# Performance work log

Hardware: AMD Instinct MI355X
Metric: run time of the kernel (lower is better)

## Reference

```python
import jax, jax.numpy as jnp
import numpy as np

N = 100_000
E = 1_000_000
D = 64
NORM_FACTOR = 100.0
LN_EPS = 1e-5


def setup_inputs() -> dict:
    key = jax.random.key(0)
    ks = jax.random.split(key, 8)
    h = jax.random.normal(ks[0], (N, D), dtype=jnp.float32)
    distances = jax.random.uniform(ks[1], (E, 1), dtype=jnp.float32)
    edges = jax.random.randint(ks[2], (2, E), 0, N, dtype=jnp.int64)
    node_mask = jnp.ones((N, 1), dtype=jnp.float32)
    edge_mask = jnp.ones((E, 1), dtype=jnp.float32)
    s = 1.0 / np.sqrt(D)
    W_lin = jax.random.normal(ks[3], (D, D), dtype=jnp.float32) * s
    b_lin = jnp.zeros((D,), dtype=jnp.float32)
    att_W1 = jax.random.normal(ks[4], (D, 2 * D + 1), dtype=jnp.float32) * (1.0 / np.sqrt(2 * D + 1))
    att_b1 = jnp.zeros((D,), dtype=jnp.float32)
    att_W2 = jax.random.normal(ks[5], (1, D), dtype=jnp.float32) * s
    att_b2 = jnp.zeros((1,), dtype=jnp.float32)
    ln_g = jnp.ones((D,), dtype=jnp.float32)
    ln_b = jnp.zeros((D,), dtype=jnp.float32)
    return {"h": h, "distances": distances, "edges": edges, "node_mask": node_mask,
            "edge_mask": edge_mask, "W_lin": W_lin, "b_lin": b_lin,
            "att_W1": att_W1, "att_b1": att_b1, "att_W2": att_W2, "att_b2": att_b2,
            "ln_g": ln_g, "ln_b": ln_b}


def reference(h, distances, edges, node_mask, edge_mask, W_lin, b_lin,
              att_W1, att_b1, att_W2, att_b2, ln_g, ln_b):
    # Linear projection: [N, D]
    x = h @ W_lin.T + b_lin
    row, col = edges[0], edges[1]
    x_row = x[row]          # [E, D]
    x_col = x[col]          # [E, D]
    # DenseAtt: MLP(concat(x_row, x_col, dist)) -> sigmoid -> * edge_mask
    cat = jnp.concatenate([x_row, x_col, distances], axis=1)  # [E, 2D+1]
    hdn = jax.nn.silu(cat @ att_W1.T + att_b1)                # [E, D]
    att = jax.nn.sigmoid(hdn @ att_W2.T + att_b2) * edge_mask # [E, 1]
    # Attention-weighted scatter-sum aggregation into row segments
    agg = x_col * att
    out = jax.ops.segment_sum(agg, row, num_segments=x.shape[0]) / NORM_FACTOR
    out = out + x           # residual
    # LayerNorm + activation
    mu = jnp.mean(out, axis=-1, keepdims=True)
    var = jnp.mean(jnp.square(out - mu), axis=-1, keepdims=True)
    y = (out - mu) * jax.lax.rsqrt(var + LN_EPS) * ln_g + ln_b
    return jax.nn.silu(y)
```

## Files before the change

### kernel.cpp

```cpp
#include <hip/hip_runtime.h>
#include <hip/hip_bf16.h>

#define N_NODES 100000
#define N_EDGES 1000000
#define DIM 64
#define NORM_INV 0.01f
#define LN_EPS 1e-5f
#define N_TILES 6250
#define PROJ_BLOCKS 1563
#define N_BUCKETS 782
#define NB_PAD 800
#define SC_EDGES 4096
#define SC_BLOCKS 245
#define OFS_STRIDE 784
#define L2E 1.4426950408889634f
#define LN2 0.6931471805599453f
#define CAP 2560

typedef __attribute__((ext_vector_type(8))) short short8;
typedef __attribute__((ext_vector_type(4))) float f32x4;

__device__ __forceinline__ unsigned short f2bf(float f) {
    union { float f; unsigned u; } x; x.f = f;
    unsigned r = x.u + 0x7FFFu + ((x.u >> 16) & 1u);
    return (unsigned short)(r >> 16);
}
__device__ __forceinline__ float bf2f(unsigned short s) {
    union { unsigned u; float f; } x; x.u = ((unsigned)s) << 16; return x.f;
}

__global__ __launch_bounds__(256) void prep_frags(
    const float* __restrict__ W, const float* __restrict__ att_W1,
    const float* __restrict__ att_b1, const float* __restrict__ att_W2,
    short8* __restrict__ whi, short8* __restrict__ wlo,
    short8* __restrict__ wa, short8* __restrict__ wb,
    float4* __restrict__ tab) {
    const int l = threadIdx.x & 63;
    const int nt = threadIdx.x >> 6;
    const int c = l & 15, q = l >> 4;
    const int n = nt * 16 + c;
#pragma unroll
    for (int ks = 0; ks < 2; ++ks) {
        const int k0 = ks * 32 + q * 8;
        short8 hi8, lo8, a8, b8;
#pragma unroll
        for (int jj = 0; jj < 8; ++jj) {
            float w = W[n * 64 + k0 + jj];
            unsigned short hh = f2bf(w);
            hi8[jj] = (short)hh;
            lo8[jj] = (short)f2bf(w - bf2f(hh));
            a8[jj] = (short)f2bf(att_W1[n * 129 + k0 + jj]);
            b8[jj] = (short)f2bf(att_W1[n * 129 + 64 + k0 + jj]);
        }
        const int idx = (nt * 2 + ks) * 64 + l;
        whi[idx] = hi8; wlo[idx] = lo8; wa[idx] = a8; wb[idx] = b8;
    }
    if (threadIdx.x < 64) {
        const int f = threadIdx.x;
        tab[f] = make_float4(att_W2[f] * LN2, att_W1[f * 129 + 128] * L2E,
                             att_b1[f] * L2E, 0.f);
    }
}

__global__ __launch_bounds__(256) void proj_scatter(
    const float* __restrict__ h, const float* __restrict__ bl,
    const short8* __restrict__ whi, const short8* __restrict__ wlo,
    const short8* __restrict__ wa, const short8* __restrict__ wb,
    const int* __restrict__ edges, const float* __restrict__ dist,
    const float* __restrict__ emask,
    uint2* __restrict__ srec, int* __restrict__ ofsT,
    unsigned short* __restrict__ xv, unsigned short* __restrict__ u_bf) {
    __shared__ __align__(16) char pool[39168];
    __shared__ int wsum[4];

    if (blockIdx.x >= PROJ_BLOCKS) {
        int* lh = (int*)pool;
        int* lofs = (int*)pool + NB_PAD;
        uint2* lsort = (uint2*)(pool + 6400);
        const int blk = blockIdx.x - PROJ_BLOCKS;
        const int tid = threadIdx.x;
        const int lane = tid & 63;
        const int w = tid >> 6;
        for (int i = tid; i < NB_PAD; i += 256) lh[i] = 0;
        __syncthreads();

        const int eb = blk * SC_EDGES;
        const int total = min(SC_EDGES, N_EDGES - eb);

        int rows[16], rank[16];
        uint2 recs[16];
        const int e0 = eb + tid * 16;
#pragma unroll
        for (int g = 0; g < 4; ++g) {
            const int e = e0 + g * 4;
            if (e + 4 <= N_EDGES) {
                const int4 rr = *(const int4*)(edges + e);
                const int4 cc = *(const int4*)(edges + N_EDGES + e);
                const float4 dd = *(const float4*)(dist + e);
                const float4 mm = *(const float4*)(emask + e);
                rows[g*4+0] = rr.x; rows[g*4+1] = rr.y; rows[g*4+2] = rr.z; rows[g*4+3] = rr.w;
                const int c4[4] = {cc.x, cc.y, cc.z, cc.w};
                const float d4[4] = {dd.x, dd.y, dd.z, dd.w};
                const float m4[4] = {mm.x, mm.y, mm.z, mm.w};
#pragma unroll
                for (int i = 0; i < 4; ++i) {
                    const int ii = g * 4 + i;
                    recs[ii].x = (unsigned)c4[i] | ((unsigned)(rows[ii] & 127) << 24);
                    recs[ii].y = (unsigned)f2bf(d4[i]) |
                                 ((unsigned)f2bf(m4[i] * NORM_INV) << 16);
                    rank[ii] = atomicAdd(&lh[rows[ii] >> 7], 1);
                }
            } else {
#pragma unroll
                for (int i = 0; i < 4; ++i) {
                    const int ii = g * 4 + i;
                    const int ee = e + i;
                    if (ee < N_EDGES) {
                        rows[ii] = edges[ee];
                        recs[ii].x = (unsigned)edges[N_EDGES + ee] |
                                     ((unsigned)(rows[ii] & 127) << 24);
                        recs[ii].y = (unsigned)f2bf(dist[ee]) |
                                     ((unsigned)f2bf(emask[ee] * NORM_INV) << 16);
                        rank[ii] = atomicAdd(&lh[rows[ii] >> 7], 1);
                    } else {
                        rows[ii] = -1;
                    }
                }
            }
        }
        __syncthreads();

        const int b0 = tid * 4;
        int c0 = 0, c1 = 0, c2 = 0, c3 = 0;
        if (b0 < NB_PAD) { c0 = lh[b0]; c1 = lh[b0+1]; c2 = lh[b0+2]; c3 = lh[b0+3]; }
        const int S = c0 + c1 + c2 + c3;
        int sc = S;
#pragma unroll
        for (int off = 1; off < 64; off <<= 1) {
            int u = __shfl_up(sc, off);
            if (lane >= off) sc += u;
        }
        if (lane == 63) wsum[w] = sc;
        __syncthreads();
        int wbase = 0;
        if (w > 0) wbase = wsum[0];
        if (w > 1) wbase += wsum[1];
        if (w > 2) wbase += wsum[2];
        const int excl = sc - S + wbase;
        if (b0 < NB_PAD) {
            lofs[b0] = excl;
            lofs[b0+1] = excl + c0;
            lofs[b0+2] = excl + c0 + c1;
            lofs[b0+3] = excl + c0 + c1 + c2;
        }
        __syncthreads();

#pragma unroll
        for (int i = 0; i < 16; ++i) {
            if (rows[i] >= 0) {
                const int bk = rows[i] >> 7;
                lsort[lofs[bk] + rank[i]] = recs[i];
            }
        }
        __syncthreads();

        for (int s = tid; s < total; s += 256)
            srec[(size_t)blk * SC_EDGES + s] = lsort[s];
        for (int b = tid; b < 783; b += 256)
            ofsT[blk * OFS_STRIDE + b] = lofs[b];
        return;
    }

    const int tid = threadIdx.x;
    {
        uint4* l4 = (uint4*)pool;
        const uint4* g0 = (const uint4*)whi;
        const uint4* g1 = (const uint4*)wlo;
        const uint4* g2 = (const uint4*)wa;
        const uint4* g3 = (const uint4*)wb;
        l4[tid]        = g0[tid];       l4[256 + tid]  = g0[256 + tid];
        l4[512 + tid]  = g1[tid];       l4[768 + tid]  = g1[256 + tid];
        l4[1024 + tid] = g2[tid];       l4[1280 + tid] = g2[256 + tid];
        l4[1536 + tid] = g3[tid];       l4[1792 + tid] = g3[256 + tid];
    }
    __syncthreads();
    const short8* Lwhi = (const short8*)pool;
    const short8* Lwlo = Lwhi + 512;
    const short8* Lwa  = Lwhi + 1024;
    const short8* Lwb  = Lwhi + 1536;

    const int lane = tid & 63;
    const int wv = tid >> 6;
    const int c = lane & 15, q = lane >> 4;
    const int tile = blockIdx.x * 4 + wv;
    const bool valid = (tile < N_TILES);
    const int n0 = valid ? tile * 16 : 0;

    float bias[4];
#pragma unroll
    for (int nt = 0; nt < 4; ++nt) bias[nt] = bl[nt * 16 + c];

    short8 Ahi[2], Alo[2];
#pragma unroll
    for (int ks = 0; ks < 2; ++ks) {
        const float* hp = h + (size_t)(n0 + c) * 64 + ks * 32 + q * 8;
        f32x4 p0 = *(const f32x4*)hp;
        f32x4 p1 = *(const f32x4*)(hp + 4);
        short8 hi8, lo8;
#pragma unroll
        for (int jj = 0; jj < 4; ++jj) {
            unsigned short hh = f2bf(p0[jj]);
            hi8[jj] = (short)hh; lo8[jj] = (short)f2bf(p0[jj] - bf2f(hh));
            unsigned short h2 = f2bf(p1[jj]);
            hi8[4 + jj] = (short)h2; lo8[4 + jj] = (short)f2bf(p1[jj] - bf2f(h2));
        }
        Ahi[ks] = hi8; Alo[ks] = lo8;
    }

    f32x4 xacc[4] = {{0,0,0,0},{0,0,0,0},{0,0,0,0},{0,0,0,0}};
#pragma unroll
    for (int ks = 0; ks < 2; ++ks)
#pragma unroll
        for (int nt = 0; nt < 4; ++nt) {
            const short8 fhi = Lwhi[(nt * 2 + ks) * 64 + lane];
            const short8 flo = Lwlo[(nt * 2 + ks) * 64 + lane];
            xacc[nt] = __builtin_amdgcn_mfma_f32_16x16x32_bf16(Ahi[ks], fhi, xacc[nt], 0, 0, 0);
            xacc[nt] = __builtin_amdgcn_mfma_f32_16x16x32_bf16(Ahi[ks], flo, xacc[nt], 0, 0, 0);
            xacc[nt] = __builtin_amdgcn_mfma_f32_16x16x32_bf16(Alo[ks], fhi, xacc[nt], 0, 0, 0);
        }

    __syncthreads();

    unsigned short* lw = (unsigned short*)pool + wv * (16 * 72);
#pragma unroll
    for (int r = 0; r < 4; ++r) {
        const int node = n0 + q * 4 + r;
        unsigned short xb[4];
#pragma unroll
        for (int nt = 0; nt < 4; ++nt) {
            unsigned short v16 = f2bf(xacc[nt][r] + bias[nt]);
            xb[nt] = v16;
            lw[(q * 4 + r) * 72 + nt * 16 + c] = v16;
        }
        if (valid) {
            uint2 pk;
            pk.x = (unsigned)xb[0] | ((unsigned)xb[1] << 16);
            pk.y = (unsigned)xb[2] | ((unsigned)xb[3] << 16);
            *(uint2*)(xv + (size_t)node * 128 + c * 8) = pk;
        }
    }

    short8 Ax[2];
#pragma unroll
    for (int ks = 0; ks < 2; ++ks)
        Ax[ks] = *(const short8*)&lw[c * 72 + ks * 32 + q * 8];

    f32x4 uacc[4] = {{0,0,0,0},{0,0,0,0},{0,0,0,0},{0,0,0,0}};
    f32x4 vacc[4] = {{0,0,0,0},{0,0,0,0},{0,0,0,0},{0,0,0,0}};
#pragma unroll
    for (int ks = 0; ks < 2; ++ks)
#pragma unroll
        for (int nt = 0; nt < 4; ++nt) {
            const short8 fa = Lwa[(nt * 2 + ks) * 64 + lane];
            const short8 fb = Lwb[(nt * 2 + ks) * 64 + lane];
            uacc[nt] = __builtin_amdgcn_mfma_f32_16x16x32_bf16(Ax[ks], fa, uacc[nt], 0, 0, 0);
            vacc[nt] = __builtin_amdgcn_mfma_f32_16x16x32_bf16(Ax[ks], fb, vacc[nt], 0, 0, 0);
        }
    if (valid) {
#pragma unroll
        for (int r = 0; r < 4; ++r) {
            const int node = n0 + q * 4 + r;
            uint2 pu;
            pu.x = (unsigned)f2bf(uacc[0][r] * L2E) | ((unsigned)f2bf(uacc[1][r] * L2E) << 16);
            pu.y = (unsigned)f2bf(uacc[2][r] * L2E) | ((unsigned)f2bf(uacc[3][r] * L2E) << 16);
            *(uint2*)(u_bf + (size_t)node * 64 + c * 4) = pu;
            uint2 pk;
            pk.x = (unsigned)f2bf(vacc[0][r] * L2E) | ((unsigned)f2bf(vacc[1][r] * L2E) << 16);
            pk.y = (unsigned)f2bf(vacc[2][r] * L2E) | ((unsigned)f2bf(vacc[3][r] * L2E) << 16);
            *(uint2*)(xv + (size_t)node * 128 + c * 8 + 4) = pk;
        }
    }
}

__global__ __launch_bounds__(512, 4) void agg_fused(
    const uint2* __restrict__ srec, const int* __restrict__ ofsT,
    const unsigned short* __restrict__ xv, const unsigned short* __restrict__ u_bf,
    const float4* __restrict__ tab, const float* __restrict__ att_b2,
    const float* __restrict__ ln_g, const float* __restrict__ ln_b,
    float* __restrict__ out) {
    __shared__ __align__(16) uint2 lrecs[CAP + 16];
    __shared__ int hist[128];
    __shared__ int rst[129];
    __shared__ int cur[128];
    __shared__ int sst[256];
    __shared__ int dbase[257];
    __shared__ int wsum4[4];
    __shared__ int wtot;

    const int b = blockIdx.x;
    const int tid = threadIdx.x;
    const int lane = tid & 63;
    const int wv = tid >> 6;

    if (tid < 128) hist[tid] = 0;

    int stv = 0, len = 0, sc0 = 0;
    if (tid < 256) {
        if (tid < SC_BLOCKS) {
            stv = ofsT[tid * OFS_STRIDE + b];
            len = ofsT[tid * OFS_STRIDE + b + 1] - stv;
        }
        sst[tid] = stv;
        sc0 = len;
#pragma unroll
        for (int off = 1; off < 64; off <<= 1) {
            int u = __shfl_up(sc0, off);
            if (lane >= off) sc0 += u;
        }
        if (lane == 63) wsum4[wv] = sc0;
    }
    __syncthreads();
    if (tid < 256) {
        int wbase = 0;
        if (wv > 0) wbase = wsum4[0];
        if (wv > 1) wbase += wsum4[1];
        if (wv > 2) wbase += wsum4[2];
        dbase[tid] = wbase + sc0 - len;
        if (tid == 255) dbase[256] = wbase + sc0;
    }
    __syncthreads();
    const int cnt = dbase[245];

    for (int m = tid; m < cnt; m += 512) {
        int lo = 0, hi = 245;
        while (hi - lo > 1) {
            const int mid = (lo + hi) >> 1;
            if (dbase[mid] <= m) lo = mid; else hi = mid;
        }
        const unsigned key =
            ((const unsigned*)srec)[2 * ((size_t)lo * SC_EDGES + sst[lo] + (m - dbase[lo]))];
        atomicAdd(&hist[key >> 24], 1);
    }
    __syncthreads();

    int c = 0, p = 0, sc = 0;
    if (tid < 128) {
        c = hist[tid];
        p = (c + 3) & ~3;
        sc = p;
#pragma unroll
        for (int off = 1; off < 64; off <<= 1) {
            int u = __shfl_up(sc, off);
            if (lane >= off) sc += u;
        }
        if (tid == 63) wtot = sc;
    }
    __syncthreads();
    if (tid < 128) {
        if (tid >= 64) sc += wtot;
        const int excl = sc - p;
        rst[tid] = excl;
        cur[tid] = excl;
        uint2 z; z.x = 0; z.y = 0;
        for (int i = c; i < p; ++i) lrecs[excl + i] = z;
        if (tid == 127) {
            rst[128] = excl + p;
            for (int i = 0; i < 16; ++i) lrecs[excl + p + i] = z;
        }
    }
    __syncthreads();

    for (int m = tid; m < cnt; m += 512) {
        int lo = 0, hi = 245;
        while (hi - lo > 1) {
            const int mid = (lo + hi) >> 1;
            if (dbase[mid] <= m) lo = mid; else hi = mid;
        }
        uint2 rec = srec[(size_t)lo * SC_EDGES + sst[lo] + (m - dbase[lo])];
        const int lr = (int)(rec.x >> 24);
        rec.x &= 0x00FFFFFFu;
        lrecs[atomicAdd(&cur[lr], 1)] = rec;
    }
    __syncthreads();

    const int j = lane & 15;
    const int sl = lane >> 4;
    const float4 t0 = tab[j], t1 = tab[j + 16], t2 = tab[j + 32], t3 = tab[j + 48];
    const float b2L = att_b2[0] * L2E;
    const float gg = ln_g[lane], bb = ln_b[lane];
    const unsigned* xvu = (const unsigned*)xv;

#pragma unroll 1
    for (int k = 0; k < 16; ++k) {
        const int lrw = wv + 8 * k;
        const int r = b * 128 + lrw;
        if (r >= N_NODES) break;

        const uint2 uu = *(const uint2*)(u_bf + (size_t)r * 64 + j * 4);
        const float base0 = __uint_as_float(uu.x << 16) + t0.z;
        const float base1 = __uint_as_float(uu.x & 0xffff0000u) + t1.z;
        const float base2 = __uint_as_float(uu.y << 16) + t2.z;
        const float base3 = __uint_as_float(uu.y & 0xffff0000u) + t3.z;

        const int s0 = rst[lrw];
        const int e1 = rst[lrw + 1];

        float a0 = 0.f, a1 = 0.f, a2 = 0.f, a3 = 0.f;
        if (e1 > s0) {
            uint2 recA = lrecs[s0 + sl];
            uint4 xvA = *(const uint4*)(xvu + (size_t)recA.x * 64 + j * 4);
            for (int e = s0; e < e1; e += 4) {
                const uint2 recB = lrecs[e + 4 + sl];
                const uint4 xvB = *(const uint4*)(xvu + (size_t)recB.x * 64 + j * 4);

                const float dist = __uint_as_float(recA.y << 16);
                const float emN = __uint_as_float(recA.y & 0xffff0000u);
                const float x0 = __uint_as_float(xvA.x << 16);
                const float x1 = __uint_as_float(xvA.x & 0xffff0000u);
                const float x2 = __uint_as_float(xvA.y << 16);
                const float x3 = __uint_as_float(xvA.y & 0xffff0000u);
                const float v0 = __uint_as_float(xvA.z << 16);
                const float v1 = __uint_as_float(xvA.z & 0xffff0000u);
                const float v2 = __uint_as_float(xvA.w << 16);
                const float v3 = __uint_as_float(xvA.w & 0xffff0000u);
                float pv = 0.f, pre, sg;
                pre = fmaf(dist, t0.y, base0) + v0;
                sg = __builtin_amdgcn_rcpf(1.f + __builtin_amdgcn_exp2f(-pre));
                pv = fmaf(pre * sg, t0.x, pv);
                pre = fmaf(dist, t1.y, base1) + v1;
                sg = __builtin_amdgcn_rcpf(1.f + __builtin_amdgcn_exp2f(-pre));
                pv = fmaf(pre * sg, t1.x, pv);
                pre = fmaf(dist, t2.y, base2) + v2;
                sg = __builtin_amdgcn_rcpf(1.f + __builtin_amdgcn_exp2f(-pre));
                pv = fmaf(pre * sg, t2.x, pv);
                pre = fmaf(dist, t3.y, base3) + v3;
                sg = __builtin_amdgcn_rcpf(1.f + __builtin_amdgcn_exp2f(-pre));
                pv = fmaf(pre * sg, t3.x, pv);
                pv += __shfl_xor(pv, 1); pv += __shfl_xor(pv, 2);
                pv += __shfl_xor(pv, 4); pv += __shfl_xor(pv, 8);
                const float sp = fmaf(pv, L2E, b2L);
                const float att =
                    emN * __builtin_amdgcn_rcpf(1.f + __builtin_amdgcn_exp2f(-sp));
                a0 = fmaf(att, x0, a0); a1 = fmaf(att, x1, a1);
                a2 = fmaf(att, x2, a2); a3 = fmaf(att, x3, a3);
                recA = recB; xvA = xvB;
            }
        }
        a0 += __shfl_xor(a0, 16); a0 += __shfl_xor(a0, 32);
        a1 += __shfl_xor(a1, 16); a1 += __shfl_xor(a1, 32);
        a2 += __shfl_xor(a2, 16); a2 += __shfl_xor(a2, 32);
        a3 += __shfl_xor(a3, 16); a3 += __shfl_xor(a3, 32);

        const uint2 xr = *(const uint2*)(xvu + (size_t)r * 64 + j * 4);
        const float o0 = __uint_as_float(xr.x << 16) + a0;
        const float o1 = __uint_as_float(xr.x & 0xffff0000u) + a1;
        const float o2 = __uint_as_float(xr.y << 16) + a2;
        const float o3 = __uint_as_float(xr.y & 0xffff0000u) + a3;

        float ssum = o0 + o1 + o2 + o3;
        ssum += __shfl_xor(ssum, 1); ssum += __shfl_xor(ssum, 2);
        ssum += __shfl_xor(ssum, 4); ssum += __shfl_xor(ssum, 8);
        const float mu = ssum * (1.f / 64.f);
        const float d0 = o0 - mu, d1 = o1 - mu, d2 = o2 - mu, d3 = o3 - mu;
        float vs = d0 * d0 + d1 * d1 + d2 * d2 + d3 * d3;
        vs += __shfl_xor(vs, 1); vs += __shfl_xor(vs, 2);
        vs += __shfl_xor(vs, 4); vs += __shfl_xor(vs, 8);
        const float rstd = rsqrtf(vs * (1.f / 64.f) + LN_EPS);

        const float dk = (sl == 0) ? d0 : (sl == 1) ? d1 : (sl == 2) ? d2 : d3;
        const float y = fmaf(dk * rstd, gg, bb);
        out[(size_t)r * 64 + lane] =
            y * __builtin_amdgcn_rcpf(1.f + __builtin_amdgcn_exp2f(-y * L2E));
    }
}

extern "C" void kernel_launch(void* const* d_in, const int* in_sizes, int n_in,
                              void* d_out, int out_size, void* d_ws, size_t ws_size,
                              hipStream_t stream) {
    const float* h      = (const float*)d_in[0];
    const float* dist   = (const float*)d_in[1];
    const int*   edges  = (const int*)d_in[2];
    const float* emask  = (const float*)d_in[4];
    const float* W_lin  = (const float*)d_in[5];
    const float* b_lin  = (const float*)d_in[6];
    const float* att_W1 = (const float*)d_in[7];
    const float* att_b1 = (const float*)d_in[8];
    const float* att_W2 = (const float*)d_in[9];
    const float* att_b2 = (const float*)d_in[10];
    const float* ln_g   = (const float*)d_in[11];
    const float* ln_b   = (const float*)d_in[12];
    float* out = (float*)d_out;

    char* ws = (char*)d_ws;
    unsigned short* xv   = (unsigned short*)ws;
    unsigned short* u_bf = (unsigned short*)(ws + 25600000);
    uint2* srec          = (uint2*)(ws + 38400000);
    int* ofsT            = (int*)(ws + 46428160);
    float4* tab          = (float4*)(ws + 47196480);
    short8* whi          = (short8*)(ws + 47197504);
    short8* wlo          = (short8*)(ws + 47205696);
    short8* wa           = (short8*)(ws + 47213888);
    short8* wb           = (short8*)(ws + 47222080);

    prep_frags<<<1, 256, 0, stream>>>(W_lin, att_W1, att_b1, att_W2,
                                      whi, wlo, wa, wb, tab);
    proj_scatter<<<PROJ_BLOCKS + SC_BLOCKS, 256, 0, stream>>>(
        h, b_lin, whi, wlo, wa, wb, edges, dist, emask, srec, ofsT, xv, u_bf);
    agg_fused<<<N_BUCKETS, 512, 0, stream>>>(srec, ofsT, xv, u_bf,
                                             tab, att_b2, ln_g, ln_b, out);
}
```

Measured before the change: 201.0 us.

## Fold weight prep into projection kernel, reorder scatter blocks, cache gathered records

Removes the separate single-block prep_frags launch. Each projection block now converts the weights to bf16 hi/lo fragments directly into shared memory, and each aggregation block builds the attention table in LDS. Scatter blocks are moved to the front of the grid so they get scheduled first. The aggregation kernel keeps up to five gathered edge records in registers across the histogram pass instead of re-reading srec with a second binary search. The trade-off is that every projection block redoes the weight conversion, and register pressure rises from holding the five records.

```diff
diff --git a/kernel.cpp b/kernel.cpp
--- a/kernel.cpp
+++ b/kernel.cpp
@@ -29,43 +29,9 @@
     union { unsigned u; float f; } x; x.u = ((unsigned)s) << 16; return x.f;
 }
 
-__global__ __launch_bounds__(256) void prep_frags(
-    const float* __restrict__ W, const float* __restrict__ att_W1,
-    const float* __restrict__ att_b1, const float* __restrict__ att_W2,
-    short8* __restrict__ whi, short8* __restrict__ wlo,
-    short8* __restrict__ wa, short8* __restrict__ wb,
-    float4* __restrict__ tab) {
-    const int l = threadIdx.x & 63;
-    const int nt = threadIdx.x >> 6;
-    const int c = l & 15, q = l >> 4;
-    const int n = nt * 16 + c;
-#pragma unroll
-    for (int ks = 0; ks < 2; ++ks) {
-        const int k0 = ks * 32 + q * 8;
-        short8 hi8, lo8, a8, b8;
-#pragma unroll
-        for (int jj = 0; jj < 8; ++jj) {
-            float w = W[n * 64 + k0 + jj];
-            unsigned short hh = f2bf(w);
-            hi8[jj] = (short)hh;
-            lo8[jj] = (short)f2bf(w - bf2f(hh));
-            a8[jj] = (short)f2bf(att_W1[n * 129 + k0 + jj]);
-            b8[jj] = (short)f2bf(att_W1[n * 129 + 64 + k0 + jj]);
-        }
-        const int idx = (nt * 2 + ks) * 64 + l;
-        whi[idx] = hi8; wlo[idx] = lo8; wa[idx] = a8; wb[idx] = b8;
-    }
-    if (threadIdx.x < 64) {
-        const int f = threadIdx.x;
-        tab[f] = make_float4(att_W2[f] * LN2, att_W1[f * 129 + 128] * L2E,
-                             att_b1[f] * L2E, 0.f);
-    }
-}
-
 __global__ __launch_bounds__(256) void proj_scatter(
     const float* __restrict__ h, const float* __restrict__ bl,
-    const short8* __restrict__ whi, const short8* __restrict__ wlo,
-    const short8* __restrict__ wa, const short8* __restrict__ wb,
+    const float* __restrict__ W, const float* __restrict__ att_W1,
     const int* __restrict__ edges, const float* __restrict__ dist,
     const float* __restrict__ emask,
     uint2* __restrict__ srec, int* __restrict__ ofsT,
@@ -73,11 +39,11 @@
     __shared__ __align__(16) char pool[39168];
     __shared__ int wsum[4];
 
-    if (blockIdx.x >= PROJ_BLOCKS) {
+    if (blockIdx.x < SC_BLOCKS) {
         int* lh = (int*)pool;
         int* lofs = (int*)pool + NB_PAD;
         uint2* lsort = (uint2*)(pool + 6400);
-        const int blk = blockIdx.x - PROJ_BLOCKS;
+        const int blk = blockIdx.x;
         const int tid = threadIdx.x;
         const int lane = tid & 63;
         const int w = tid >> 6;
@@ -172,16 +138,33 @@
     }
 
     const int tid = threadIdx.x;
+    const int lane = tid & 63;
+    const int wv = tid >> 6;
+    const int c = lane & 15, q = lane >> 4;
+
     {
-        uint4* l4 = (uint4*)pool;
-        const uint4* g0 = (const uint4*)whi;
-        const uint4* g1 = (const uint4*)wlo;
-        const uint4* g2 = (const uint4*)wa;
-        const uint4* g3 = (const uint4*)wb;
-        l4[tid]        = g0[tid];       l4[256 + tid]  = g0[256 + tid];
-        l4[512 + tid]  = g1[tid];       l4[768 + tid]  = g1[256 + tid];
-        l4[1024 + tid] = g2[tid];       l4[1280 + tid] = g2[256 + tid];
-        l4[1536 + tid] = g3[tid];       l4[1792 + tid] = g3[256 + tid];
+        short8* Lwhi_w = (short8*)pool;
+        short8* Lwlo_w = Lwhi_w + 512;
+        short8* Lwa_w  = Lwhi_w + 1024;
+        short8* Lwb_w  = Lwhi_w + 1536;
+        const int nt_b = tid >> 6;
+        const int n_b = nt_b * 16 + c;
+#pragma unroll
+        for (int ks = 0; ks < 2; ++ks) {
+            const int k0 = ks * 32 + q * 8;
+            short8 hi8, lo8, a8, b8;
+#pragma unroll
+            for (int jj = 0; jj < 8; ++jj) {
+                float w = W[n_b * 64 + k0 + jj];
+                unsigned short hh = f2bf(w);
+                hi8[jj] = (short)hh;
+                lo8[jj] = (short)f2bf(w - bf2f(hh));
+                a8[jj] = (short)f2bf(att_W1[n_b * 129 + k0 + jj]);
+                b8[jj] = (short)f2bf(att_W1[n_b * 129 + 64 + k0 + jj]);
+            }
+            const int idx = (nt_b * 2 + ks) * 64 + lane;
+            Lwhi_w[idx] = hi8; Lwlo_w[idx] = lo8; Lwa_w[idx] = a8; Lwb_w[idx] = b8;
+        }
     }
     __syncthreads();
     const short8* Lwhi = (const short8*)pool;
@@ -189,10 +172,7 @@
     const short8* Lwa  = Lwhi + 1024;
     const short8* Lwb  = Lwhi + 1536;
 
-    const int lane = tid & 63;
-    const int wv = tid >> 6;
-    const int c = lane & 15, q = lane >> 4;
-    const int tile = blockIdx.x * 4 + wv;
+    const int tile = (blockIdx.x - SC_BLOCKS) * 4 + wv;
     const bool valid = (tile < N_TILES);
     const int n0 = valid ? tile * 16 : 0;
 
@@ -285,10 +265,12 @@
 __global__ __launch_bounds__(512, 4) void agg_fused(
     const uint2* __restrict__ srec, const int* __restrict__ ofsT,
     const unsigned short* __restrict__ xv, const unsigned short* __restrict__ u_bf,
-    const float4* __restrict__ tab, const float* __restrict__ att_b2,
+    const float* __restrict__ att_W1, const float* __restrict__ att_b1,
+    const float* __restrict__ att_W2, const float* __restrict__ att_b2,
     const float* __restrict__ ln_g, const float* __restrict__ ln_b,
     float* __restrict__ out) {
     __shared__ __align__(16) uint2 lrecs[CAP + 16];
+    __shared__ float4 ltab[64];
     __shared__ int hist[128];
     __shared__ int rst[129];
     __shared__ int cur[128];
@@ -303,6 +285,11 @@
     const int wv = tid >> 6;
 
     if (tid < 128) hist[tid] = 0;
+    if (tid >= 448) {
+        const int f = tid - 448;
+        ltab[f] = make_float4(att_W2[f] * LN2, att_W1[f * 129 + 128] * L2E,
+                              att_b1[f] * L2E, 0.f);
+    }
 
     int stv = 0, len = 0, sc0 = 0;
     if (tid < 256) {
@@ -331,16 +318,29 @@
     __syncthreads();
     const int cnt = dbase[245];
 
-    for (int m = tid; m < cnt; m += 512) {
-        int lo = 0, hi = 245;
-        while (hi - lo > 1) {
-            const int mid = (lo + hi) >> 1;
-            if (dbase[mid] <= m) lo = mid; else hi = mid;
-        }
-        const unsigned key =
-            ((const unsigned*)srec)[2 * ((size_t)lo * SC_EDGES + sst[lo] + (m - dbase[lo]))];
-        atomicAdd(&hist[key >> 24], 1);
-    }
+    uint2 rec0, rec1, rec2, rec3, rec4;
+    int lr0 = -1, lr1 = -1, lr2 = -1, lr3 = -1, lr4 = -1;
+#define GATHER(I, RC, LR)                                                     \
+    {                                                                         \
+        const int m = tid + I * 512;                                          \
+        if (m < cnt) {                                                        \
+            int lo = 0, hi = 245;                                             \
+            while (hi - lo > 1) {                                             \
+                const int mid = (lo + hi) >> 1;                               \
+                if (dbase[mid] <= m) lo = mid; else hi = mid;                 \
+            }                                                                 \
+            RC = srec[(size_t)lo * SC_EDGES + sst[lo] + (m - dbase[lo])];     \
+            LR = (int)(RC.x >> 24);                                           \
+            RC.x &= 0x00FFFFFFu;                                              \
+            atomicAdd(&hist[LR], 1);                                          \
+        }                                                                     \
+    }
+    GATHER(0, rec0, lr0)
+    GATHER(1, rec1, lr1)
+    GATHER(2, rec2, lr2)
+    GATHER(3, rec3, lr3)
+    GATHER(4, rec4, lr4)
+#undef GATHER
     __syncthreads();
 
     int c = 0, p = 0, sc = 0;
@@ -370,22 +370,16 @@
     }
     __syncthreads();
 
-    for (int m = tid; m < cnt; m += 512) {
-        int lo = 0, hi = 245;
-        while (hi - lo > 1) {
-            const int mid = (lo + hi) >> 1;
-            if (dbase[mid] <= m) lo = mid; else hi = mid;
-        }
-        uint2 rec = srec[(size_t)lo * SC_EDGES + sst[lo] + (m - dbase[lo])];
-        const int lr = (int)(rec.x >> 24);
-        rec.x &= 0x00FFFFFFu;
-        lrecs[atomicAdd(&cur[lr], 1)] = rec;
-    }
+    if (lr0 >= 0) lrecs[atomicAdd(&cur[lr0], 1)] = rec0;
+    if (lr1 >= 0) lrecs[atomicAdd(&cur[lr1], 1)] = rec1;
+    if (lr2 >= 0) lrecs[atomicAdd(&cur[lr2], 1)] = rec2;
+    if (lr3 >= 0) lrecs[atomicAdd(&cur[lr3], 1)] = rec3;
+    if (lr4 >= 0) lrecs[atomicAdd(&cur[lr4], 1)] = rec4;
     __syncthreads();
 
     const int j = lane & 15;
     const int sl = lane >> 4;
-    const float4 t0 = tab[j], t1 = tab[j + 16], t2 = tab[j + 32], t3 = tab[j + 48];
+    const float4 t0 = ltab[j], t1 = ltab[j + 16], t2 = ltab[j + 32], t3 = ltab[j + 48];
     const float b2L = att_b2[0] * L2E;
     const float gg = ln_g[lane], bb = ln_b[lane];
     const unsigned* xvu = (const unsigned*)xv;
@@ -496,16 +490,10 @@
     unsigned short* u_bf = (unsigned short*)(ws + 25600000);
     uint2* srec          = (uint2*)(ws + 38400000);
     int* ofsT            = (int*)(ws + 46428160);
-    float4* tab          = (float4*)(ws + 47196480);
-    short8* whi          = (short8*)(ws + 47197504);
-    short8* wlo          = (short8*)(ws + 47205696);
-    short8* wa           = (short8*)(ws + 47213888);
-    short8* wb           = (short8*)(ws + 47222080);
-
-    prep_frags<<<1, 256, 0, stream>>>(W_lin, att_W1, att_b1, att_W2,
-                                      whi, wlo, wa, wb, tab);
-    proj_scatter<<<PROJ_BLOCKS + SC_BLOCKS, 256, 0, stream>>>(
-        h, b_lin, whi, wlo, wa, wb, edges, dist, emask, srec, ofsT, xv, u_bf);
+
+    proj_scatter<<<SC_BLOCKS + PROJ_BLOCKS, 256, 0, stream>>>(
+        h, b_lin, W_lin, att_W1, edges, dist, emask, srec, ofsT, xv, u_bf);
     agg_fused<<<N_BUCKETS, 512, 0, stream>>>(srec, ofsT, xv, u_bf,
-                                             tab, att_b2, ln_g, ln_b, out);
+                                             att_W1, att_b1, att_W2, att_b2,
+                                             ln_g, ln_b, out);
 }
```

Result: no change. 197.4 us (-1.8%).
